# Performance work log

Hardware: AMD Instinct MI355X
Metric: run time of the kernel (lower is better)

Reference implementation:

```python
import jax, jax.numpy as jnp
import numpy as np

B, N, D, H, DK, DV, R = 4, 256, 256, 8, 32, 32, 64
EPS = 1e-6


def setup_inputs() -> dict:
    key = jax.random.key(0)
    ks = jax.random.split(key, 16)
    s = D ** -0.5
    return {
        "q": jax.random.normal(ks[0], (B, N, D), jnp.float32),
        "k": jax.random.normal(ks[1], (B, N, D), jnp.float32),
        "v": jax.random.normal(ks[2], (B, N, D), jnp.float32),
        "mask": jax.random.randint(ks[3], (B, N, N), 0, 2).astype(jnp.int32),
        "link": jax.random.uniform(ks[4], (B, N, N, R), jnp.float32),
        "Wq": jax.random.normal(ks[5], (D, H * DK), jnp.float32) * s,
        "Wk": jax.random.normal(ks[6], (D, H * DK), jnp.float32) * s,
        "Wr": jax.random.normal(ks[7], (D, H * DK), jnp.float32) * s,
        "Wv": jax.random.normal(ks[8], (D, H * DV), jnp.float32) * s,
        "Wvv": jax.random.normal(ks[9], (D, H * DV), jnp.float32) * s,
        "relationE": jax.random.normal(ks[10], (R, D), jnp.float32) * s,
        "Wo": jax.random.normal(ks[11], (H * DV, D), jnp.float32) * s,
        "gamma": jnp.ones((D,), jnp.float32),
        "beta": jnp.zeros((D,), jnp.float32),
    }


def reference(q, k, v, mask, link, Wq, Wk, Wr, Wv, Wvv, relationE, Wo, gamma, beta):
    # rela_num != 0 branch of Ruleformer MultiHeadAttention (dropout = identity, eval mode).
    residual = q
    b, n, d = q.shape
    # per-head projections of X (== q == residual in this branch): [b,h,n,dk]
    Xq = (q @ Wq).reshape(b, n, H, DK).transpose(0, 2, 1, 3)
    Xk = (q @ Wk).reshape(b, n, H, DK).transpose(0, 2, 1, 3)
    Xv = (q @ Wv).reshape(b, n, H, DV).transpose(0, 2, 1, 3)

    # calcE: relation-biased scores. Rk[b,i,j,h,d] = (link @ relationE @ Wr)
    Rk = jnp.einsum('bijr,re->bije', link, relationE @ Wr).reshape(b, n, n, H, DK)
    # attn[b,h,i,j] = Xq[b,h,i] . (Xk[b,h,j] + Rk[b,i,j,h])
    attn = jnp.einsum('bhid,bhjd->bhij', Xq, Xk)
    attn = attn + jnp.einsum('bijhd,bhid->bhij', Rk, Xq)
    attn = attn / (DK ** 0.5)
    attn = jnp.where(mask[:, None, :, :] == 0, -1e9, attn)
    alpha = jax.nn.softmax(attn, axis=-1)  # [b,h,n,n]

    # calcZ: Z[b,h,i] = sum_j alpha[b,h,i,j] * (Xv[b,h,j] + Rv[b,i,j,h])
    Rv = jnp.einsum('bijr,re->bije', link, relationE @ Wvv).reshape(b, n, n, H, DV)
    Z = jnp.einsum('bhij,bhjd->bhid', alpha, Xv)
    Z = Z + jnp.einsum('bhij,bijhd->bhid', alpha, Rv)

    out = Z.transpose(0, 2, 1, 3).reshape(b, n, H * DV) @ Wo
    out = out + residual
    mu = out.mean(-1, keepdims=True)
    var = ((out - mu) ** 2).mean(-1, keepdims=True)
    out = (out - mu) * jax.lax.rsqrt(var + EPS) * gamma + beta
    return out, alpha
```

## Files before the change

kernel.cpp:

```cpp
#include <hip/hip_runtime.h>
#include <math.h>

constexpr int B_ = 4, N_ = 256, D_ = 256, H_ = 8, DK_ = 32, DV_ = 32, R_ = 64;
constexpr float SCALE_ = 0.17677669529663687f;
constexpr float EPS_ = 1e-6f;

__global__ __launch_bounds__(256) void projekev_kernel(
        const float* __restrict__ q, const float* __restrict__ Wq,
        const float* __restrict__ Wk, const float* __restrict__ Wv,
        const float* __restrict__ relE, const float* __restrict__ Wr,
        const float* __restrict__ Wvv, float* __restrict__ Xq,
        float* __restrict__ Xk, float* __restrict__ Xv,
        float* __restrict__ Ek, float* __restrict__ Ev) {
    int blk = blockIdx.x;
    int t = threadIdx.x;
    __shared__ __align__(16) float ash[32 * 65];
    __shared__ __align__(16) float bsh[32 * 64];
    const float *src, *W;
    int rowbase, cbase, ct;
    float* dstE = nullptr;
    if (blk < 192) {
        ct = blk >> 4;
        int rt = blk & 15;
        src = q; rowbase = rt * 64;
        if (ct < 4)      { W = Wq; cbase = ct * 64; }
        else if (ct < 8) { W = Wk; cbase = (ct - 4) * 64; }
        else             { W = Wv; cbase = (ct - 8) * 64; }
    } else {
        int e = blk - 192;
        src = relE; rowbase = 0; ct = -1;
        W = (e < 4) ? Wr : Wvv;
        dstE = (e < 4) ? Ek : Ev;
        cbase = (e & 3) * 64;
    }
    int ti = t >> 4, tj = t & 15;
    float acc[4][4] = {{0.f}};
    for (int kc = 0; kc < 8; ++kc) {
        __syncthreads();
#pragma unroll
        for (int kk = 0; kk < 2; ++kk) {
            int m = t + kk * 256;
            int i = m >> 3, kq = m & 7;
            float4 v = *(const float4*)(src + (size_t)(rowbase + i) * 256 + kc * 32 + kq * 4);
            ash[(kq * 4 + 0) * 65 + i] = v.x;
            ash[(kq * 4 + 1) * 65 + i] = v.y;
            ash[(kq * 4 + 2) * 65 + i] = v.z;
            ash[(kq * 4 + 3) * 65 + i] = v.w;
        }
#pragma unroll
        for (int kk = 0; kk < 2; ++kk) {
            int m = t + kk * 256;
            int k = m >> 4, j4 = m & 15;
            float4 v = *(const float4*)(W + (size_t)(kc * 32 + k) * 256 + cbase + j4 * 4);
            *(float4*)(bsh + k * 64 + j4 * 4) = v;
        }
        __syncthreads();
#pragma unroll 8
        for (int k = 0; k < 32; ++k) {
            float4 av = *(const float4*)(ash + k * 65 + ti * 4);
            float4 bv = *(const float4*)(bsh + k * 64 + tj * 4);
            acc[0][0] += av.x * bv.x; acc[0][1] += av.x * bv.y;
            acc[0][2] += av.x * bv.z; acc[0][3] += av.x * bv.w;
            acc[1][0] += av.y * bv.x; acc[1][1] += av.y * bv.y;
            acc[1][2] += av.y * bv.z; acc[1][3] += av.y * bv.w;
            acc[2][0] += av.z * bv.x; acc[2][1] += av.z * bv.y;
            acc[2][2] += av.z * bv.z; acc[2][3] += av.z * bv.w;
            acc[3][0] += av.w * bv.x; acc[3][1] += av.w * bv.y;
            acc[3][2] += av.w * bv.z; acc[3][3] += av.w * bv.w;
        }
    }
    if (dstE) {
#pragma unroll
        for (int a = 0; a < 4; ++a) {
            int row = ti * 4 + a;
            *(float4*)(dstE + (size_t)row * 256 + cbase + tj * 4) =
                make_float4(acc[a][0], acc[a][1], acc[a][2], acc[a][3]);
        }
    } else {
        float* dst = (ct < 4) ? Xq : (ct < 8) ? Xk : Xv;
        int gcol = (ct & 3) * 64 + tj * 4;
        int h = gcol >> 5, dk = gcol & 31;
#pragma unroll
        for (int a = 0; a < 4; ++a) {
            int row = rowbase + ti * 4 + a;
            int bb = row >> 8, n = row & 255;
            *(float4*)(dst + ((size_t)(bb * 8 + h) * 256 + n) * 32 + dk) =
                make_float4(acc[a][0], acc[a][1], acc[a][2], acc[a][3]);
        }
    }
}

__global__ __launch_bounds__(256) void qkT_kernel(
        const float* __restrict__ Xq, const float* __restrict__ Xk,
        const float* __restrict__ Ek, float* __restrict__ qk,
        float* __restrict__ T) {
    int x = blockIdx.x;
    int jt = x & 3, it = (x >> 2) & 3, bh = x >> 4;
    int b = bh >> 3, h = bh & 7;
    int t = threadIdx.x;
    __shared__ __align__(16) float xqsh[32 * 64];
    __shared__ __align__(16) float xksh[32 * 64];
    __shared__ __align__(16) float eksh[32 * 64];
#pragma unroll
    for (int k = 0; k < 2; ++k) {
        int m = t + k * 256;
        int i = m >> 3, dq4 = m & 7;
        float4 v = *(const float4*)(Xq + ((size_t)(bh * 256 + it * 64 + i)) * 32 + dq4 * 4);
        xqsh[(dq4 * 4 + 0) * 64 + i] = v.x;
        xqsh[(dq4 * 4 + 1) * 64 + i] = v.y;
        xqsh[(dq4 * 4 + 2) * 64 + i] = v.z;
        xqsh[(dq4 * 4 + 3) * 64 + i] = v.w;
        float4 u = *(const float4*)(Xk + ((size_t)(bh * 256 + jt * 64 + i)) * 32 + dq4 * 4);
        xksh[(dq4 * 4 + 0) * 64 + i] = u.x;
        xksh[(dq4 * 4 + 1) * 64 + i] = u.y;
        xksh[(dq4 * 4 + 2) * 64 + i] = u.z;
        xksh[(dq4 * 4 + 3) * 64 + i] = u.w;
    }
    if (jt == 0) {
        int r = t >> 2, dq = t & 3;
#pragma unroll
        for (int kk = 0; kk < 2; ++kk) {
            int dq4 = dq + kk * 4;
            float4 v = *(const float4*)(Ek + r * 256 + h * 32 + dq4 * 4);
            eksh[(dq4 * 4 + 0) * 64 + r] = v.x;
            eksh[(dq4 * 4 + 1) * 64 + r] = v.y;
            eksh[(dq4 * 4 + 2) * 64 + r] = v.z;
            eksh[(dq4 * 4 + 3) * 64 + r] = v.w;
        }
    }
    __syncthreads();
    int ti = t >> 4, tj = t & 15;
    float acc[4][4] = {{0.f}};
#pragma unroll 8
    for (int dk = 0; dk < 32; ++dk) {
        float4 av = *(const float4*)(xqsh + dk * 64 + ti * 4);
        float4 bv = *(const float4*)(xksh + dk * 64 + tj * 4);
        acc[0][0] += av.x * bv.x; acc[0][1] += av.x * bv.y;
        acc[0][2] += av.x * bv.z; acc[0][3] += av.x * bv.w;
        acc[1][0] += av.y * bv.x; acc[1][1] += av.y * bv.y;
        acc[1][2] += av.y * bv.z; acc[1][3] += av.y * bv.w;
        acc[2][0] += av.z * bv.x; acc[2][1] += av.z * bv.y;
        acc[2][2] += av.z * bv.z; acc[2][3] += av.z * bv.w;
        acc[3][0] += av.w * bv.x; acc[3][1] += av.w * bv.y;
        acc[3][2] += av.w * bv.z; acc[3][3] += av.w * bv.w;
    }
#pragma unroll
    for (int a = 0; a < 4; ++a) {
        int i = it * 64 + ti * 4 + a;
        *(float4*)(qk + ((size_t)(bh * 256 + i)) * 256 + jt * 64 + tj * 4) =
            make_float4(acc[a][0], acc[a][1], acc[a][2], acc[a][3]);
    }
    if (jt == 0) {
        float tacc[4][4] = {{0.f}};
#pragma unroll 8
        for (int dk = 0; dk < 32; ++dk) {
            float4 av = *(const float4*)(xqsh + dk * 64 + ti * 4);
            float4 ev = *(const float4*)(eksh + dk * 64 + tj * 4);
            tacc[0][0] += av.x * ev.x; tacc[0][1] += av.x * ev.y;
            tacc[0][2] += av.x * ev.z; tacc[0][3] += av.x * ev.w;
            tacc[1][0] += av.y * ev.x; tacc[1][1] += av.y * ev.y;
            tacc[1][2] += av.y * ev.z; tacc[1][3] += av.y * ev.w;
            tacc[2][0] += av.z * ev.x; tacc[2][1] += av.z * ev.y;
            tacc[2][2] += av.z * ev.z; tacc[2][3] += av.z * ev.w;
            tacc[3][0] += av.w * ev.x; tacc[3][1] += av.w * ev.y;
            tacc[3][2] += av.w * ev.z; tacc[3][3] += av.w * ev.w;
        }
#pragma unroll
        for (int a = 0; a < 4; ++a) {
            int i = it * 64 + ti * 4 + a;
            *(float4*)(T + ((size_t)(b * 256 + i)) * 512 + h * 64 + tj * 4) =
                make_float4(tacc[a][0], tacc[a][1], tacc[a][2], tacc[a][3]);
        }
    }
}

__global__ __launch_bounds__(256, 8) void biassmz_kernel(
        const float* __restrict__ link, const float* __restrict__ Tg,
        const float* __restrict__ qk, const int* __restrict__ mask,
        const float* __restrict__ Xv, const float* __restrict__ Ev,
        float* __restrict__ alpha, float* __restrict__ Z) {
    int v = ((blockIdx.x & 7) << 8) | (blockIdx.x >> 3);
    int bi = v >> 1, hg = v & 1;
    int b = bi >> 8, i = bi & 255;
    int h0 = hg * 4;
    int t = threadIdx.x;
    int lane = t & 63, g = t >> 6;

    __shared__ __align__(16) float Tsh[4 * 68];
    __shared__ __align__(16) float ashm[4 * 260];
    __shared__ __align__(16) float part[1024];
    __shared__ float redsh[32];

    float qv[4];
#pragma unroll
    for (int hh = 0; hh < 4; ++hh)
        qv[hh] = qk[((size_t)(b * 8 + h0 + hh) * 256 + i) * 256 + t];
    int mv = mask[((size_t)(b * 256 + i)) * 256 + t];
    {
        int hh = t >> 6, r = t & 63;
        Tsh[hh * 68 + r] = Tg[(size_t)bi * 512 + (h0 + hh) * 64 + r];
    }
    __syncthreads();

    float s[4] = {0.f, 0.f, 0.f, 0.f};
    {
        const float4* l4 = (const float4*)(link + ((size_t)(bi * 256 + t)) * 64);
        const float4* T4 = (const float4*)Tsh;
#pragma unroll 4
        for (int k = 0; k < 16; ++k) {
            float4 lv = l4[k];
#pragma unroll
            for (int hh = 0; hh < 4; ++hh) {
                float4 tv = T4[hh * 17 + k];
                s[hh] += lv.x * tv.x + lv.y * tv.y + lv.z * tv.z + lv.w * tv.w;
            }
        }
    }
#pragma unroll
    for (int hh = 0; hh < 4; ++hh) {
        s[hh] = (qv[hh] + s[hh]) * SCALE_;
        if (mv == 0) s[hh] = -1e9f;
    }

#pragma unroll
    for (int hh = 0; hh < 4; ++hh) {
        float v2 = s[hh];
        for (int off = 32; off > 0; off >>= 1) v2 = fmaxf(v2, __shfl_xor(v2, off));
        if (lane == 0) redsh[hh * 4 + g] = v2;
    }
    __syncthreads();
    float mx[4];
#pragma unroll
    for (int hh = 0; hh < 4; ++hh) {
        const float* rp = redsh + hh * 4;
        mx[hh] = fmaxf(fmaxf(rp[0], rp[1]), fmaxf(rp[2], rp[3]));
    }
#pragma unroll
    for (int hh = 0; hh < 4; ++hh) {
        float e = __expf(s[hh] - mx[hh]);
        s[hh] = e;
        float v2 = e;
        for (int off = 32; off > 0; off >>= 1) v2 += __shfl_xor(v2, off);
        if (lane == 0) redsh[16 + hh * 4 + g] = v2;
    }
    __syncthreads();
#pragma unroll
    for (int hh = 0; hh < 4; ++hh) {
        const float* rp = redsh + 16 + hh * 4;
        float esum = rp[0] + rp[1] + rp[2] + rp[3];
        float a = s[hh] * (1.f / esum);
        ashm[hh * 260 + t] = a;
        alpha[((size_t)(b * 8 + h0 + hh) * 256 + i) * 256 + t] = a;
    }
    __syncthreads();

    {
        float pacc[4] = {0.f, 0.f, 0.f, 0.f};
        const float* lp2 = link + ((size_t)(bi * 256 + g * 64)) * 64 + lane;
#pragma unroll 4
        for (int j4 = 0; j4 < 16; ++j4) {
            float l0 = lp2[(j4 * 4 + 0) * 64];
            float l1 = lp2[(j4 * 4 + 1) * 64];
            float l2 = lp2[(j4 * 4 + 2) * 64];
            float l3 = lp2[(j4 * 4 + 3) * 64];
#pragma unroll
            for (int hh = 0; hh < 4; ++hh) {
                float4 a = *(const float4*)(ashm + hh * 260 + g * 64 + j4 * 4);
                pacc[hh] += a.x * l0 + a.y * l1 + a.z * l2 + a.w * l3;
            }
        }
#pragma unroll
        for (int hh = 0; hh < 4; ++hh) part[g * 256 + hh * 64 + lane] = pacc[hh];
    }
    __syncthreads();
    {
        int hh = t >> 6, r = t & 63;
        Tsh[hh * 68 + r] = part[hh * 64 + r] + part[256 + hh * 64 + r] +
                           part[512 + hh * 64 + r] + part[768 + hh * 64 + r];
    }
    __syncthreads();

    {
        int c = t >> 5, o = t & 31;
        int hh = o >> 3, dv4 = o & 7;
        const float4* xv4 = (const float4*)Xv + (((size_t)(b * 8 + h0 + hh)) * 256 + c * 32) * 8 + dv4;
        const float* ap = ashm + hh * 260 + c * 32;
        float4 z = make_float4(0.f, 0.f, 0.f, 0.f);
#pragma unroll 8
        for (int j = 0; j < 32; ++j) {
            float a = ap[j];
            float4 x = xv4[j * 8];
            z.x += a * x.x; z.y += a * x.y; z.z += a * x.z; z.w += a * x.w;
        }
        const float4* ev4 = (const float4*)Ev + (c * 8) * 64 + (h0 + hh) * 8 + dv4;
        const float* sp = Tsh + hh * 68 + c * 8;
#pragma unroll
        for (int r = 0; r < 8; ++r) {
            float sv = sp[r];
            float4 e = ev4[r * 64];
            z.x += sv * e.x; z.y += sv * e.y; z.z += sv * e.z; z.w += sv * e.w;
        }
        ((float4*)part)[c * 32 + o] = z;
    }
    __syncthreads();
    if (t < 128) {
        float zv = 0.f;
#pragma unroll
        for (int c = 0; c < 8; ++c) zv += part[c * 128 + t];
        Z[(size_t)bi * 256 + hg * 128 + t] = zv;
    }
}

__global__ __launch_bounds__(256) void out_kernel(
        const float* __restrict__ Z, const float* __restrict__ Wo,
        const float* __restrict__ q, const float* __restrict__ gamma,
        const float* __restrict__ beta, float* __restrict__ out) {
    int row0 = blockIdx.x * 2;
    int t = threadIdx.x;
    __shared__ __align__(16) float zsh[512];
    __shared__ float redsh[16];
    zsh[t] = Z[(size_t)row0 * 256 + t];
    zsh[256 + t] = Z[(size_t)row0 * 256 + 256 + t];
    __syncthreads();
    float a0 = q[(size_t)row0 * 256 + t];
    float a1 = q[(size_t)(row0 + 1) * 256 + t];
    for (int d4 = 0; d4 < 64; ++d4) {
        float w0 = Wo[(d4 * 4 + 0) * 256 + t];
        float w1 = Wo[(d4 * 4 + 1) * 256 + t];
        float w2 = Wo[(d4 * 4 + 2) * 256 + t];
        float w3 = Wo[(d4 * 4 + 3) * 256 + t];
        float4 z0v = *(const float4*)(zsh + d4 * 4);
        float4 z1v = *(const float4*)(zsh + 256 + d4 * 4);
        a0 += z0v.x * w0 + z0v.y * w1 + z0v.z * w2 + z0v.w * w3;
        a1 += z1v.x * w0 + z1v.y * w1 + z1v.z * w2 + z1v.w * w3;
    }
    int lane = t & 63, wv = t >> 6;
    float acc2[2] = {a0, a1};
#pragma unroll
    for (int rr = 0; rr < 2; ++rr) {
        float v = acc2[rr], v2 = acc2[rr] * acc2[rr];
        for (int off = 32; off > 0; off >>= 1) {
            v += __shfl_xor(v, off);
            v2 += __shfl_xor(v2, off);
        }
        if (lane == 0) {
            redsh[rr * 8 + wv] = v;
            redsh[rr * 8 + 4 + wv] = v2;
        }
    }
    __syncthreads();
#pragma unroll
    for (int rr = 0; rr < 2; ++rr) {
        float sum = redsh[rr * 8 + 0] + redsh[rr * 8 + 1] + redsh[rr * 8 + 2] + redsh[rr * 8 + 3];
        float sum2 = redsh[rr * 8 + 4] + redsh[rr * 8 + 5] + redsh[rr * 8 + 6] + redsh[rr * 8 + 7];
        float mu = sum * (1.f / 256.f);
        float var = sum2 * (1.f / 256.f) - mu * mu;
        float dev = acc2[rr] - mu;
        out[(size_t)(row0 + rr) * 256 + t] = dev * rsqrtf(var + EPS_) * gamma[t] + beta[t];
    }
}

extern "C" void kernel_launch(void* const* d_in, const int* in_sizes, int n_in,
                              void* d_out, int out_size, void* d_ws, size_t ws_size,
                              hipStream_t stream) {
    const float* q     = (const float*)d_in[0];
    const int*   mask  = (const int*)d_in[3];
    const float* link  = (const float*)d_in[4];
    const float* Wq    = (const float*)d_in[5];
    const float* Wk    = (const float*)d_in[6];
    const float* Wr    = (const float*)d_in[7];
    const float* Wv    = (const float*)d_in[8];
    const float* Wvv   = (const float*)d_in[9];
    const float* relE  = (const float*)d_in[10];
    const float* Wo    = (const float*)d_in[11];
    const float* gamma = (const float*)d_in[12];
    const float* beta  = (const float*)d_in[13];

    float* out   = (float*)d_out;
    float* alpha = out + B_ * N_ * D_;

    float* ws = (float*)d_ws;
    float* Ek    = ws;
    float* Ev    = Ek + 16384;
    float* Xq    = Ev + 16384;
    float* Xk    = Xq + 262144;
    float* Xv    = Xk + 262144;
    float* T     = Xv + 262144;
    float* qkbuf = T + 524288;
    float* Zb    = qkbuf + 2097152;

    projekev_kernel<<<200, 256, 0, stream>>>(q, Wq, Wk, Wv, relE, Wr, Wvv,
                                             Xq, Xk, Xv, Ek, Ev);
    qkT_kernel<<<512, 256, 0, stream>>>(Xq, Xk, Ek, qkbuf, T);
    biassmz_kernel<<<2048, 256, 0, stream>>>(link, T, qkbuf, mask, Xv, Ev,
                                             alpha, Zb);
    out_kernel<<<512, 256, 0, stream>>>(Zb, Wo, q, gamma, beta, out);
}
```

Before: 192.2 us.

## Split softmax-bias kernel over key chunks with unnormalised exp and separate finalize

The fused score/softmax/Z kernel is split into two. The first kernel processes 64-key chunks for all 8 heads, stages the link tile in shared memory so it is read from global memory once instead of twice, writes unnormalised exponentials, and produces partial link-weighted sums and partial Z. A new finalize kernel reduces the partials, normalises alpha in place, and applies the Ev projection. This removes the duplicate link traffic and the in-block max reduction. It adds an extra read and write pass over alpha plus partial buffers. Dropping the max subtraction risks overflow for large scores, and masked rows underflow to zero.

```diff
diff --git a/kernel.cpp b/kernel.cpp
--- a/kernel.cpp
+++ b/kernel.cpp
@@ -174,140 +174,154 @@
     }
 }
 
-__global__ __launch_bounds__(256, 8) void biassmz_kernel(
+__global__ __launch_bounds__(256) void expsz_kernel(
         const float* __restrict__ link, const float* __restrict__ Tg,
         const float* __restrict__ qk, const int* __restrict__ mask,
-        const float* __restrict__ Xv, const float* __restrict__ Ev,
-        float* __restrict__ alpha, float* __restrict__ Z) {
-    int v = ((blockIdx.x & 7) << 8) | (blockIdx.x >> 3);
-    int bi = v >> 1, hg = v & 1;
+        const float* __restrict__ Xv, float* __restrict__ alphaU,
+        float* __restrict__ Spart, float* __restrict__ Zpart) {
+    int v = ((blockIdx.x & 7) << 9) | (blockIdx.x >> 3);
+    int bi = v >> 2, jc = v & 3;
     int b = bi >> 8, i = bi & 255;
-    int h0 = hg * 4;
+    int t = threadIdx.x;
+    int g = t >> 6, jl = t & 63;
+    int j0 = jc * 64;
+    int h0 = g * 2, h1 = g * 2 + 1;
+
+    __shared__ __align__(16) float linksh[64 * 68];
+    __shared__ __align__(16) float Tsh[8 * 68];
+    __shared__ __align__(16) float expsh[8 * 66];
+    __shared__ __align__(16) float4 zsh[4 * 64];
+
+    {
+        const float4* lp4 = (const float4*)(link + ((size_t)bi * 256 + j0) * 64);
+#pragma unroll
+        for (int k = 0; k < 4; ++k) {
+            int m = t + k * 256;
+            int j = m >> 4, rq = m & 15;
+            *(float4*)(linksh + j * 68 + rq * 4) = lp4[m];
+        }
+    }
+    for (int m = t; m < 512; m += 256)
+        Tsh[(m >> 6) * 68 + (m & 63)] = Tg[(size_t)bi * 512 + m];
+    float qv0 = qk[((size_t)(b * 8 + h0) * 256 + i) * 256 + j0 + jl];
+    float qv1 = qk[((size_t)(b * 8 + h1) * 256 + i) * 256 + j0 + jl];
+    int mv = mask[((size_t)(b * 256 + i)) * 256 + j0 + jl];
+    __syncthreads();
+
+    float s0 = 0.f, s1 = 0.f;
+    {
+        const float4* lr = (const float4*)(linksh + jl * 68);
+        const float4* t0 = (const float4*)(Tsh + h0 * 68);
+        const float4* t1 = (const float4*)(Tsh + h1 * 68);
+#pragma unroll
+        for (int rq = 0; rq < 16; ++rq) {
+            float4 lv = lr[rq];
+            float4 a0 = t0[rq], a1 = t1[rq];
+            s0 += lv.x * a0.x + lv.y * a0.y + lv.z * a0.z + lv.w * a0.w;
+            s1 += lv.x * a1.x + lv.y * a1.y + lv.z * a1.z + lv.w * a1.w;
+        }
+    }
+    s0 = (qv0 + s0) * SCALE_;
+    s1 = (qv1 + s1) * SCALE_;
+    if (mv == 0) { s0 = -1e9f; s1 = -1e9f; }
+    float e0 = __expf(s0), e1 = __expf(s1);
+    expsh[h0 * 66 + jl] = e0;
+    expsh[h1 * 66 + jl] = e1;
+    alphaU[((size_t)(b * 8 + h0) * 256 + i) * 256 + j0 + jl] = e0;
+    alphaU[((size_t)(b * 8 + h1) * 256 + i) * 256 + j0 + jl] = e1;
+    __syncthreads();
+
+    {
+        float acc0 = 0.f, acc1 = 0.f;
+        const float* ls = linksh + jl;
+        const float* e0p = expsh + h0 * 66;
+        const float* e1p = expsh + h1 * 66;
+#pragma unroll 8
+        for (int j = 0; j < 64; ++j) {
+            float lv = ls[j * 68];
+            acc0 += e0p[j] * lv;
+            acc1 += e1p[j] * lv;
+        }
+        float* sp = Spart + ((size_t)bi * 4 + jc) * 512;
+        sp[h0 * 64 + jl] = acc0;
+        sp[h1 * 64 + jl] = acc1;
+    }
+
+    {
+        int o = jl;
+        int h = o >> 3, dv4 = o & 7;
+        const float4* xv4 = (const float4*)Xv +
+            (((size_t)(b * 8 + h)) * 256 + j0 + g * 16) * 8 + dv4;
+        const float* ep = expsh + h * 66 + g * 16;
+        float4 z = make_float4(0.f, 0.f, 0.f, 0.f);
+#pragma unroll
+        for (int j = 0; j < 16; ++j) {
+            float a = ep[j];
+            float4 x = xv4[j * 8];
+            z.x += a * x.x; z.y += a * x.y; z.z += a * x.z; z.w += a * x.w;
+        }
+        zsh[g * 64 + o] = z;
+    }
+    __syncthreads();
+    if (t < 64) {
+        float4 z0 = zsh[t], z1 = zsh[64 + t], z2 = zsh[128 + t], z3 = zsh[192 + t];
+        float4 z = make_float4(z0.x + z1.x + z2.x + z3.x,
+                               z0.y + z1.y + z2.y + z3.y,
+                               z0.z + z1.z + z2.z + z3.z,
+                               z0.w + z1.w + z2.w + z3.w);
+        *(float4*)(Zpart + ((size_t)bi * 4 + jc) * 256 + t * 4) = z;
+    }
+}
+
+__global__ __launch_bounds__(256) void finz_kernel(
+        const float* __restrict__ Spart, const float* __restrict__ Zpart,
+        const float* __restrict__ Ev, float* __restrict__ alpha,
+        float* __restrict__ Z) {
+    int bi = blockIdx.x;
+    int b = bi >> 8, i = bi & 255;
     int t = threadIdx.x;
     int lane = t & 63, g = t >> 6;
-
-    __shared__ __align__(16) float Tsh[4 * 68];
-    __shared__ __align__(16) float ashm[4 * 260];
-    __shared__ __align__(16) float part[1024];
+    __shared__ __align__(16) float Ssh[8 * 68];
+    __shared__ float invsh[8];
     __shared__ float redsh[32];
 
-    float qv[4];
-#pragma unroll
-    for (int hh = 0; hh < 4; ++hh)
-        qv[hh] = qk[((size_t)(b * 8 + h0 + hh) * 256 + i) * 256 + t];
-    int mv = mask[((size_t)(b * 256 + i)) * 256 + t];
+    for (int m = t; m < 512; m += 256) {
+        float sv = Spart[((size_t)bi * 4 + 0) * 512 + m] +
+                   Spart[((size_t)bi * 4 + 1) * 512 + m] +
+                   Spart[((size_t)bi * 4 + 2) * 512 + m] +
+                   Spart[((size_t)bi * 4 + 3) * 512 + m];
+        Ssh[(m >> 6) * 68 + (m & 63)] = sv;
+    }
+    float a[8];
+#pragma unroll
+    for (int k = 0; k < 8; ++k)
+        a[k] = alpha[((size_t)(b * 8 + k) * 256 + i) * 256 + t];
+    float zq = Zpart[((size_t)bi * 4 + 0) * 256 + t] +
+               Zpart[((size_t)bi * 4 + 1) * 256 + t] +
+               Zpart[((size_t)bi * 4 + 2) * 256 + t] +
+               Zpart[((size_t)bi * 4 + 3) * 256 + t];
+#pragma unroll
+    for (int k = 0; k < 8; ++k) {
+        float v = a[k];
+        for (int off = 32; off > 0; off >>= 1) v += __shfl_xor(v, off);
+        if (lane == 0) redsh[k * 4 + g] = v;
+    }
+    __syncthreads();
+    if (t < 8)
+        invsh[t] = 1.f / (redsh[t * 4] + redsh[t * 4 + 1] +
+                          redsh[t * 4 + 2] + redsh[t * 4 + 3]);
+    __syncthreads();
+#pragma unroll
+    for (int k = 0; k < 8; ++k)
+        alpha[((size_t)(b * 8 + k) * 256 + i) * 256 + t] = a[k] * invsh[k];
     {
-        int hh = t >> 6, r = t & 63;
-        Tsh[hh * 68 + r] = Tg[(size_t)bi * 512 + (h0 + hh) * 64 + r];
-    }
-    __syncthreads();
-
-    float s[4] = {0.f, 0.f, 0.f, 0.f};
-    {
-        const float4* l4 = (const float4*)(link + ((size_t)(bi * 256 + t)) * 64);
-        const float4* T4 = (const float4*)Tsh;
+        int h = t >> 5, dv = t & 31;
+        float acc = 0.f;
+        const float* sp = Ssh + h * 68;
+        const float* evp = Ev + h * 32 + dv;
 #pragma unroll 4
-        for (int k = 0; k < 16; ++k) {
-            float4 lv = l4[k];
-#pragma unroll
-            for (int hh = 0; hh < 4; ++hh) {
-                float4 tv = T4[hh * 17 + k];
-                s[hh] += lv.x * tv.x + lv.y * tv.y + lv.z * tv.z + lv.w * tv.w;
-            }
-        }
-    }
-#pragma unroll
-    for (int hh = 0; hh < 4; ++hh) {
-        s[hh] = (qv[hh] + s[hh]) * SCALE_;
-        if (mv == 0) s[hh] = -1e9f;
-    }
-
-#pragma unroll
-    for (int hh = 0; hh < 4; ++hh) {
-        float v2 = s[hh];
-        for (int off = 32; off > 0; off >>= 1) v2 = fmaxf(v2, __shfl_xor(v2, off));
-        if (lane == 0) redsh[hh * 4 + g] = v2;
-    }
-    __syncthreads();
-    float mx[4];
-#pragma unroll
-    for (int hh = 0; hh < 4; ++hh) {
-        const float* rp = redsh + hh * 4;
-        mx[hh] = fmaxf(fmaxf(rp[0], rp[1]), fmaxf(rp[2], rp[3]));
-    }
-#pragma unroll
-    for (int hh = 0; hh < 4; ++hh) {
-        float e = __expf(s[hh] - mx[hh]);
-        s[hh] = e;
-        float v2 = e;
-        for (int off = 32; off > 0; off >>= 1) v2 += __shfl_xor(v2, off);
-        if (lane == 0) redsh[16 + hh * 4 + g] = v2;
-    }
-    __syncthreads();
-#pragma unroll
-    for (int hh = 0; hh < 4; ++hh) {
-        const float* rp = redsh + 16 + hh * 4;
-        float esum = rp[0] + rp[1] + rp[2] + rp[3];
-        float a = s[hh] * (1.f / esum);
-        ashm[hh * 260 + t] = a;
-        alpha[((size_t)(b * 8 + h0 + hh) * 256 + i) * 256 + t] = a;
-    }
-    __syncthreads();
-
-    {
-        float pacc[4] = {0.f, 0.f, 0.f, 0.f};
-        const float* lp2 = link + ((size_t)(bi * 256 + g * 64)) * 64 + lane;
-#pragma unroll 4
-        for (int j4 = 0; j4 < 16; ++j4) {
-            float l0 = lp2[(j4 * 4 + 0) * 64];
-            float l1 = lp2[(j4 * 4 + 1) * 64];
-            float l2 = lp2[(j4 * 4 + 2) * 64];
-            float l3 = lp2[(j4 * 4 + 3) * 64];
-#pragma unroll
-            for (int hh = 0; hh < 4; ++hh) {
-                float4 a = *(const float4*)(ashm + hh * 260 + g * 64 + j4 * 4);
-                pacc[hh] += a.x * l0 + a.y * l1 + a.z * l2 + a.w * l3;
-            }
-        }
-#pragma unroll
-        for (int hh = 0; hh < 4; ++hh) part[g * 256 + hh * 64 + lane] = pacc[hh];
-    }
-    __syncthreads();
-    {
-        int hh = t >> 6, r = t & 63;
-        Tsh[hh * 68 + r] = part[hh * 64 + r] + part[256 + hh * 64 + r] +
-                           part[512 + hh * 64 + r] + part[768 + hh * 64 + r];
-    }
-    __syncthreads();
-
-    {
-        int c = t >> 5, o = t & 31;
-        int hh = o >> 3, dv4 = o & 7;
-        const float4* xv4 = (const float4*)Xv + (((size_t)(b * 8 + h0 + hh)) * 256 + c * 32) * 8 + dv4;
-        const float* ap = ashm + hh * 260 + c * 32;
-        float4 z = make_float4(0.f, 0.f, 0.f, 0.f);
-#pragma unroll 8
-        for (int j = 0; j < 32; ++j) {
-            float a = ap[j];
-            float4 x = xv4[j * 8];
-            z.x += a * x.x; z.y += a * x.y; z.z += a * x.z; z.w += a * x.w;
-        }
-        const float4* ev4 = (const float4*)Ev + (c * 8) * 64 + (h0 + hh) * 8 + dv4;
-        const float* sp = Tsh + hh * 68 + c * 8;
-#pragma unroll
-        for (int r = 0; r < 8; ++r) {
-            float sv = sp[r];
-            float4 e = ev4[r * 64];
-            z.x += sv * e.x; z.y += sv * e.y; z.z += sv * e.z; z.w += sv * e.w;
-        }
-        ((float4*)part)[c * 32 + o] = z;
-    }
-    __syncthreads();
-    if (t < 128) {
-        float zv = 0.f;
-#pragma unroll
-        for (int c = 0; c < 8; ++c) zv += part[c * 128 + t];
-        Z[(size_t)bi * 256 + hg * 128 + t] = zv;
+        for (int r = 0; r < 64; ++r) acc += sp[r] * evp[r * 256];
+        Z[(size_t)bi * 256 + t] = (zq + acc) * invsh[h];
     }
 }
 
@@ -387,12 +401,14 @@
     float* Xv    = Xk + 262144;
     float* T     = Xv + 262144;
     float* qkbuf = T + 524288;
-    float* Zb    = qkbuf + 2097152;
+    float* Spart = qkbuf + 2097152;
+    float* Zpart = Spart + 2097152;
 
     projekev_kernel<<<200, 256, 0, stream>>>(q, Wq, Wk, Wv, relE, Wr, Wvv,
                                              Xq, Xk, Xv, Ek, Ev);
     qkT_kernel<<<512, 256, 0, stream>>>(Xq, Xk, Ek, qkbuf, T);
-    biassmz_kernel<<<2048, 256, 0, stream>>>(link, T, qkbuf, mask, Xv, Ev,
-                                             alpha, Zb);
-    out_kernel<<<512, 256, 0, stream>>>(Zb, Wo, q, gamma, beta, out);
-}
+    expsz_kernel<<<4096, 256, 0, stream>>>(link, T, qkbuf, mask, Xv,
+                                           alpha, Spart, Zpart);
+    finz_kernel<<<1024, 256, 0, stream>>>(Spart, Zpart, Ev, alpha, Xq);
+    out_kernel<<<512, 256, 0, stream>>>(Xq, Wo, q, gamma, beta, out);
+}
```

Measured after the change: 186.5 us. 1.03x faster.
